# Kernel optimization log

Measured on AMD Instinct MI355X. Metric: run time of the kernel, lower is better.

Reference implementation:

```python
import jax, jax.numpy as jnp
import numpy as np

B, C, H, W = 32, 192, 32, 32
CH, STRIDE = 8, 2
FEAT = CH * (H // STRIDE) * (W // STRIDE)  # 8*16*16 = 2048


def setup_inputs() -> dict:
    key = jax.random.key(0)
    ks = jax.random.split(key, 7)
    inp = jax.random.normal(ks[0], (B, C, H, W), jnp.float32)
    w_left_out = jax.random.normal(ks[1], (B, C, H, W), jnp.float32)
    conv_w = jax.random.normal(ks[2], (CH, C, 3, 3), jnp.float32) * 0.05
    conv_b = jnp.zeros((CH,), jnp.float32)
    # small scale keeps diag(U) moderate so exp(s) stays finite
    lin_w = jax.random.normal(ks[3], (C * C, FEAT), jnp.float32) * 0.01
    lin_b = jax.random.normal(ks[4], (C * C,), jnp.float32) * 0.1
    s_sign = jnp.sign(jax.random.normal(ks[5], (C,), jnp.float32))
    return dict(inp=inp, w_left_out=w_left_out, conv_w=conv_w, conv_b=conv_b,
                lin_w=lin_w, lin_b=lin_b, s_sign=s_sign)


def _cond_net(x, conv_w, conv_b, lin_w, lin_b):
    # Conv2d(C->CH, k=3, stride=2, pad=1) + ReLU + Flatten + Linear(FEAT -> C*C)
    h = jax.lax.conv_general_dilated(
        x, conv_w, window_strides=(STRIDE, STRIDE), padding=((1, 1), (1, 1)),
        dimension_numbers=('NCHW', 'OIHW', 'NCHW'))
    h = jax.nn.relu(h + conv_b[None, :, None, None])
    return h.reshape(x.shape[0], -1) @ lin_w.T + lin_b  # [B, C*C]


def reference(inp, w_left_out, conv_w, conv_b, lin_w, lin_b, s_sign):
    b, c, height, width = inp.shape
    cond = _cond_net(w_left_out, conv_w, conv_b, lin_w, lin_b)
    mats = cond.reshape(b, c, c)
    # batched LU: a = p @ l @ u (scipy convention, unit-diag l)
    p, l, u = jax.vmap(jax.scipy.linalg.lu)(mats)
    s = jnp.diagonal(u, axis1=1, axis2=2)          # [B, C] raw diag(U)
    eye = jnp.eye(c, dtype=inp.dtype)
    l_full = jnp.tril(l, -1) + eye                  # l * l_mask + I
    u_full = jnp.triu(u, 1) + (s_sign[None, :] * jnp.exp(s))[..., None] * eye
    weight = p @ l_full @ u_full                    # [B, C, C]
    # batched 1x1 conv == per-sample GEMM over spatial positions
    out = jnp.einsum('bij,bjhw->bihw', weight, inp)
    log_w = jnp.mean(jnp.sum(s, axis=1))            # sum(w_s) averaged over batch
    log_det = (height * width) * log_w
    return out, log_det
```

## Files before the change

### kernel.cpp

```cpp
#include <hip/hip_runtime.h>
#include <math.h>


#define NFEAT 2048
#define NN    36864

__global__ __launch_bounds__(256) void conv_kernel(const float* __restrict__ w,
                                                   const float* __restrict__ cw,
                                                   float* __restrict__ hpart) {
  int blk = blockIdx.x;
  int b = blk >> 2, cs = blk & 3;
  int tid = threadIdx.x;
  int oy = tid >> 4, ox = tid & 15;
  __shared__ float wlds[8 * 48 * 9];
  for (int idx = tid; idx < 8 * 48 * 9; idx += 256) {
    int ch = idx / 432, rem = idx - ch * 432;
    int c = rem / 9, kk = rem - c * 9;
    wlds[idx] = cw[ch * 1728 + (cs * 48 + c) * 9 + kk];
  }
  __syncthreads();
  float acc[8];
#pragma unroll
  for (int ch = 0; ch < 8; ++ch) acc[ch] = 0.f;
  const float* img0 = w + (((size_t)b * 192 + cs * 48) << 10);
  for (int c = 0; c < 48; ++c) {
    const float* img = img0 + ((size_t)c << 10);
    float iv[9];
#pragma unroll
    for (int ky = 0; ky < 3; ++ky)
#pragma unroll
      for (int kx = 0; kx < 3; ++kx) {
        int iy = 2 * oy - 1 + ky, ix = 2 * ox - 1 + kx;
        bool ok = (iy >= 0) & (iy < 32) & (ix >= 0) & (ix < 32);
        iv[ky * 3 + kx] = ok ? img[iy * 32 + ix] : 0.f;
      }
#pragma unroll
    for (int ch = 0; ch < 8; ++ch) {
      const float* wp = &wlds[(ch * 48 + c) * 9];
      float s = acc[ch];
#pragma unroll
      for (int t = 0; t < 9; ++t) s = fmaf(iv[t], wp[t], s);
      acc[ch] = s;
    }
  }
  size_t base = ((size_t)(cs * 32 + b) << 11) + tid;
#pragma unroll
  for (int ch = 0; ch < 8; ++ch) hpart[base + (ch << 8)] = acc[ch];
}

__global__ __launch_bounds__(256) void hreduce_kernel(const float* __restrict__ hpart,
                                                      const float* __restrict__ cb,
                                                      float* __restrict__ h_t) {
  int g = blockIdx.x * 256 + threadIdx.x;
  int k = g & 2047, b = g >> 11;
  float s = 0.f;
#pragma unroll
  for (int cs = 0; cs < 4; ++cs) s += hpart[(((size_t)(cs * 32 + b)) << 11) + k];
  s += cb[k >> 8];
  s = fmaxf(s, 0.f);
  h_t[((size_t)k << 5) + b] = s;
}

__global__ __launch_bounds__(256) void linear_kernel(const float* __restrict__ h_t,
                                                     const float* __restrict__ lw,
                                                     const float* __restrict__ lb,
                                                     float* __restrict__ mats) {
  __shared__ float Wbuf[64 * 68];
  __shared__ float Hbuf[64 * 36];
  int tid = threadIdx.x;
  int n0 = blockIdx.x << 6;
  int half = tid >> 5;
  int bb = tid & 31;
  int nb = half << 3;
  float accq0[8], accq1[8], accq2[8], accq3[8];
#pragma unroll
  for (int j = 0; j < 8; ++j) { accq0[j] = 0.f; accq1[j] = 0.f; accq2[j] = 0.f; accq3[j] = 0.f; }

#define LIN_CHUNK(ACC)                                                         \
  {                                                                            \
    int koff = kc << 6;                                                        \
    _Pragma("unroll") for (int j = 0; j < 4; ++j) {                            \
      int f = tid + (j << 8);                                                  \
      int row = f >> 4, c4 = (f & 15) << 2;                                    \
      *(float4*)(Wbuf + row * 68 + c4) =                                       \
          *(const float4*)(lw + (size_t)(n0 + row) * 2048 + koff + c4);        \
    }                                                                          \
    _Pragma("unroll") for (int j = 0; j < 2; ++j) {                            \
      int f = tid + (j << 8);                                                  \
      int kr = f >> 3, b4 = (f & 7) << 2;                                      \
      *(float4*)(Hbuf + kr * 36 + b4) =                                        \
          *(const float4*)(h_t + (((size_t)(koff + kr)) << 5) + b4);           \
    }                                                                          \
    __syncthreads();                                                           \
    _Pragma("unroll 4") for (int k4 = 0; k4 < 16; ++k4) {                      \
      int kk = k4 << 2;                                                        \
      float h0 = Hbuf[(kk + 0) * 36 + bb];                                     \
      float h1 = Hbuf[(kk + 1) * 36 + bb];                                     \
      float h2 = Hbuf[(kk + 2) * 36 + bb];                                     \
      float h3 = Hbuf[(kk + 3) * 36 + bb];                                     \
      _Pragma("unroll") for (int j = 0; j < 8; ++j) {                          \
        float4 w4 = *(const float4*)(Wbuf + (nb + j) * 68 + kk);               \
        float s = ACC[j];                                                      \
        s = fmaf(w4.x, h0, s);                                                 \
        s = fmaf(w4.y, h1, s);                                                 \
        s = fmaf(w4.z, h2, s);                                                 \
        s = fmaf(w4.w, h3, s);                                                 \
        ACC[j] = s;                                                            \
      }                                                                        \
    }                                                                          \
    __syncthreads();                                                           \
  }

  for (int kc = 0; kc < 8; ++kc)  LIN_CHUNK(accq0)
  for (int kc = 8; kc < 16; ++kc) LIN_CHUNK(accq1)
  for (int kc = 16; kc < 24; ++kc) LIN_CHUNK(accq2)
  for (int kc = 24; kc < 32; ++kc) LIN_CHUNK(accq3)
#undef LIN_CHUNK

  float o[8];
#pragma unroll
  for (int j = 0; j < 8; ++j)
    o[j] = ((accq0[j] + accq1[j]) + accq2[j]) + accq3[j] + lb[n0 + nb + j];
  float* mp = mats + (size_t)bb * NN + n0 + nb;
  *(float4*)(mp + 0) = make_float4(o[0], o[1], o[2], o[3]);
  *(float4*)(mp + 4) = make_float4(o[4], o[5], o[6], o[7]);
}

#define CAT_(A, B) A##B
#define CAT(A, B) CAT_(A, B)
#define PR_0(R) CAT(pA, R).x
#define PR_1(R) CAT(pA, R).y
#define PR_2(R) CAT(pA, R).z
#define PR_3(R) CAT(pA, R).w
#define PR_4(R) CAT(pB, R).x
#define PR_5(R) CAT(pB, R).y
#define PR_6(R) CAT(pB, R).z
#define PR_7(R) CAT(pB, R).w
#define PR(R, K) CAT(PR_, K)(R)
#define UU_0 uA.x
#define UU_1 uA.y
#define UU_2 uA.z
#define UU_3 uA.w
#define UU_4 uB.x
#define UU_5 uB.y
#define UU_6 uB.z
#define UU_7 uB.w
#define UU(K) CAT(UU_, K)
#define UPDJ(R, J) PR(R, J) = fmaf(-m, UU(J), PR(R, J));
#define TAIL_0(R) UPDJ(R,1) UPDJ(R,2) UPDJ(R,3) UPDJ(R,4) UPDJ(R,5) UPDJ(R,6) UPDJ(R,7)
#define TAIL_1(R) UPDJ(R,2) UPDJ(R,3) UPDJ(R,4) UPDJ(R,5) UPDJ(R,6) UPDJ(R,7)
#define TAIL_2(R) UPDJ(R,3) UPDJ(R,4) UPDJ(R,5) UPDJ(R,6) UPDJ(R,7)
#define TAIL_3(R) UPDJ(R,4) UPDJ(R,5) UPDJ(R,6) UPDJ(R,7)
#define TAIL_4(R) UPDJ(R,5) UPDJ(R,6) UPDJ(R,7)
#define TAIL_5(R) UPDJ(R,6) UPDJ(R,7)
#define TAIL_6(R) UPDJ(R,7)
#define TAIL_7(R)
#define UPDROW(R, KK, kg)                                                      \
  if (CAT(lg, R) > (kg)) {                                                     \
    float m = PR(R, KK) * recip;                                               \
    PR(R, KK) = m;                                                             \
    CAT(TAIL_, KK)(R)                                                          \
  }
#define PSTEP(KK) {                                                            \
  const int kg = kpP + KK;                                                     \
  float bv = -1.f; int br = 0x7fffffff;                                        \
  { float v = fabsf(PR(0,KK)); if (lg0 >= kg && (v > bv || (v == bv && lg0 < br))) { bv = v; br = lg0; } } \
  { float v = fabsf(PR(1,KK)); if (lg1 >= kg && (v > bv || (v == bv && lg1 < br))) { bv = v; br = lg1; } } \
  { float v = fabsf(PR(2,KK)); if (lg2 >= kg && (v > bv || (v == bv && lg2 < br))) { bv = v; br = lg2; } } \
  for (int msk = 1; msk <= 32; msk <<= 1) {                                    \
    float ov = __shfl_xor(bv, msk, 64);                                        \
    int obr = __shfl_xor(br, msk, 64);                                         \
    if (ov > bv || (ov == bv && obr < br)) { bv = ov; br = obr; }              \
  }                                                                            \
  bool own0 = (lg0 == br), own1 = (lg1 == br), own2 = (lg2 == br);             \
  float4 sA = own1 ? pA1 : (own2 ? pA2 : pA0);                                 \
  float4 sB = own1 ? pB1 : (own2 ? pB2 : pB0);                                 \
  int owner = (int)__ffsll(__ballot(own0 | own1 | own2)) - 1;                  \
  float4 uA, uB;                                                               \
  uA.x = __shfl(sA.x, owner); uA.y = __shfl(sA.y, owner);                      \
  uA.z = __shfl(sA.z, owner); uA.w = __shfl(sA.w, owner);                      \
  uB.x = __shfl(sB.x, owner); uB.y = __shfl(sB.y, owner);                      \
  uB.z = __shfl(sB.z, owner); uB.w = __shfl(sB.w, owner);                      \
  float piv = UU(KK);                                                          \
  float recip = 1.0f / piv;                                                    \
  if (tid == 0) {                                                              \
    diagU[kg] = piv;                                                           \
    int t0 = rowmap[kg], t1 = rowmap[br];                                      \
    rowmap[kg] = t1; rowmap[br] = t0;                                          \
  }                                                                            \
  lg0 = (lg0 == kg) ? br : ((lg0 == br) ? kg : lg0);                           \
  lg1 = (lg1 == kg) ? br : ((lg1 == br) ? kg : lg1);                           \
  lg2 = (lg2 == kg) ? br : ((lg2 == br) ? kg : lg2);                           \
  UPDROW(0, KK, kg)                                                            \
  UPDROW(1, KK, kg)                                                            \
  UPDROW(2, KK, kg)                                                            \
}
#define FMA4(D, M, S) {                                                        \
  float mm = (M);                                                              \
  D.x = fmaf(-mm, S.x, D.x); D.y = fmaf(-mm, S.y, D.y);                        \
  D.z = fmaf(-mm, S.z, D.z); D.w = fmaf(-mm, S.w, D.w);                        \
}
#define PANEL(KPV) {                                                           \
  const int kpP = (KPV);                                                       \
  const int pcP = kpP >> 2;                                                    \
  float4 pA0 = As4[tid * 49 + pcP],         pB0 = As4[tid * 49 + pcP + 1];     \
  float4 pA1 = As4[(tid + 64) * 49 + pcP],  pB1 = As4[(tid + 64) * 49 + pcP + 1]; \
  float4 pA2 = As4[(tid + 128) * 49 + pcP], pB2 = As4[(tid + 128) * 49 + pcP + 1]; \
  PSTEP(0) PSTEP(1) PSTEP(2) PSTEP(3) PSTEP(4) PSTEP(5) PSTEP(6) PSTEP(7)     \
  As4[tid * 49 + pcP] = pA0;         As4[tid * 49 + pcP + 1] = pB0;            \
  As4[(tid + 64) * 49 + pcP] = pA1;  As4[(tid + 64) * 49 + pcP + 1] = pB1;     \
  As4[(tid + 128) * 49 + pcP] = pA2; As4[(tid + 128) * 49 + pcP + 1] = pB2;    \
}

__global__ __launch_bounds__(768, 1) void lu_kernel(float* __restrict__ A0,
                                                    const float* __restrict__ ssign,
                                                    float* __restrict__ ssum) {
  __shared__ float4 As4[192 * 49];
  __shared__ int rowmap[192];
  __shared__ float diagU[192];
  __shared__ float4 dval4[48];
  float* dvalf = (float*)dval4;
  int b = blockIdx.x;
  int tid = threadIdx.x;
  float* __restrict__ A = A0 + (size_t)b * NN;

#pragma unroll
  for (int j = 0; j < 12; ++j) {
    int chunk = tid + 768 * j;
    int row = chunk / 48, q = chunk - row * 48;
    As4[row * 49 + q] = *(const float4*)(A + row * 192 + 4 * q);
  }
  for (int i = tid; i < 192; i += 768) rowmap[i] = i;
  __syncthreads();

  int lg0 = tid, lg1 = tid + 64, lg2 = tid + 128;

  if (tid < 64) { PANEL(0) }
  __syncthreads();

  const int qg = tid >> 4;
  const int slot = tid & 15;

  for (int p = 0; p < 23; ++p) {
    const int kp = p << 3;
    const int pc = kp >> 2;
    const int qp1 = pc + 2;

    if (tid >= qp1 && tid < 48) {
      const int q = tid;
      const int ur0 = rowmap[kp + 0], ur1 = rowmap[kp + 1];
      const int ur2 = rowmap[kp + 2], ur3 = rowmap[kp + 3];
      const int ur4 = rowmap[kp + 4], ur5 = rowmap[kp + 5];
      const int ur6 = rowmap[kp + 6], ur7 = rowmap[kp + 7];
      float4 u40 = As4[ur0 * 49 + q], u41 = As4[ur1 * 49 + q];
      float4 u42 = As4[ur2 * 49 + q], u43 = As4[ur3 * 49 + q];
      float4 u44 = As4[ur4 * 49 + q], u45 = As4[ur5 * 49 + q];
      float4 u46 = As4[ur6 * 49 + q], u47 = As4[ur7 * 49 + q];
      { float4 la = As4[ur1 * 49 + pc];
        FMA4(u41, la.x, u40) }
      { float4 la = As4[ur2 * 49 + pc];
        FMA4(u42, la.x, u40) FMA4(u42, la.y, u41) }
      { float4 la = As4[ur3 * 49 + pc];
        FMA4(u43, la.x, u40) FMA4(u43, la.y, u41) FMA4(u43, la.z, u42) }
      { float4 la = As4[ur4 * 49 + pc];
        FMA4(u44, la.x, u40) FMA4(u44, la.y, u41) FMA4(u44, la.z, u42) FMA4(u44, la.w, u43) }
      { float4 la = As4[ur5 * 49 + pc]; float4 lb2 = As4[ur5 * 49 + pc + 1];
        FMA4(u45, la.x, u40) FMA4(u45, la.y, u41) FMA4(u45, la.z, u42) FMA4(u45, la.w, u43)
        FMA4(u45, lb2.x, u44) }
      { float4 la = As4[ur6 * 49 + pc]; float4 lb2 = As4[ur6 * 49 + pc + 1];
        FMA4(u46, la.x, u40) FMA4(u46, la.y, u41) FMA4(u46, la.z, u42) FMA4(u46, la.w, u43)
        FMA4(u46, lb2.x, u44) FMA4(u46, lb2.y, u45) }
      { float4 la = As4[ur7 * 49 + pc]; float4 lb2 = As4[ur7 * 49 + pc + 1];
        FMA4(u47, la.x, u40) FMA4(u47, la.y, u41) FMA4(u47, la.z, u42) FMA4(u47, la.w, u43)
        FMA4(u47, lb2.x, u44) FMA4(u47, lb2.y, u45) FMA4(u47, lb2.z, u46) }
      As4[ur0 * 49 + q] = u40; As4[ur1 * 49 + q] = u41;
      As4[ur2 * 49 + q] = u42; As4[ur3 * 49 + q] = u43;
      As4[ur4 * 49 + q] = u44; As4[ur5 * 49 + q] = u45;
      As4[ur6 * 49 + q] = u46; As4[ur7 * 49 + q] = u47;
    }
    __syncthreads();

    {
      const int col = qp1 + (tid >= 384 ? 1 : 0);
      const int rsl = tid - (tid >= 384 ? 384 : 0);
      const int s = kp + 8 + rsl;
      if (s < 192) {
        const int ua0 = rowmap[kp + 0], ua1 = rowmap[kp + 1];
        const int ua2 = rowmap[kp + 2], ua3 = rowmap[kp + 3];
        const int ua4 = rowmap[kp + 4], ua5 = rowmap[kp + 5];
        const int ua6 = rowmap[kp + 6], ua7 = rowmap[kp + 7];
        float4 u40 = As4[ua0 * 49 + col], u41 = As4[ua1 * 49 + col];
        float4 u42 = As4[ua2 * 49 + col], u43 = As4[ua3 * 49 + col];
        float4 u44 = As4[ua4 * 49 + col], u45 = As4[ua5 * 49 + col];
        float4 u46 = As4[ua6 * 49 + col], u47 = As4[ua7 * 49 + col];
        int phys = rowmap[s];
        float4 la = As4[phys * 49 + pc];
        float4 lb2 = As4[phys * 49 + pc + 1];
        float4 c = As4[phys * 49 + col];
        FMA4(c, la.x, u40) FMA4(c, la.y, u41) FMA4(c, la.z, u42) FMA4(c, la.w, u43)
        FMA4(c, lb2.x, u44) FMA4(c, lb2.y, u45) FMA4(c, lb2.z, u46) FMA4(c, lb2.w, u47)
        As4[phys * 49 + col] = c;
      }
    }
    int php0, php1, php2, php3, php4, php5, php6, php7, php8, php9, php10, php11;
#define SNAP(I) CAT(php, I) = rowmap[slot + (I << 4)];
    SNAP(0) SNAP(1) SNAP(2) SNAP(3) SNAP(4) SNAP(5) SNAP(6)
    SNAP(7) SNAP(8) SNAP(9) SNAP(10) SNAP(11)
#undef SNAP
    __syncthreads();

    if (tid < 64) {
      PANEL(kp + 8)
    } else if (qg >= qp1 + 2) {
      const int q = qg;
      const int ub0 = rowmap[kp + 0], ub1 = rowmap[kp + 1];
      const int ub2 = rowmap[kp + 2], ub3 = rowmap[kp + 3];
      const int ub4 = rowmap[kp + 4], ub5 = rowmap[kp + 5];
      const int ub6 = rowmap[kp + 6], ub7 = rowmap[kp + 7];
      float4 u40 = As4[ub0 * 49 + q], u41 = As4[ub1 * 49 + q];
      float4 u42 = As4[ub2 * 49 + q], u43 = As4[ub3 * 49 + q];
      float4 u44 = As4[ub4 * 49 + q], u45 = As4[ub5 * 49 + q];
      float4 u46 = As4[ub6 * 49 + q], u47 = As4[ub7 * 49 + q];
#define GEMMROW(I) {                                                           \
      int s = slot + (I << 4);                                                 \
      if (s >= kp + 8) {                                                       \
        int phys = CAT(php, I);                                                \
        float4 la = As4[phys * 49 + pc];                                       \
        float4 lb2 = As4[phys * 49 + pc + 1];                                  \
        float4 c = As4[phys * 49 + q];                                         \
        FMA4(c, la.x, u40) FMA4(c, la.y, u41) FMA4(c, la.z, u42) FMA4(c, la.w, u43) \
        FMA4(c, lb2.x, u44) FMA4(c, lb2.y, u45) FMA4(c, lb2.z, u46) FMA4(c, lb2.w, u47) \
        As4[phys * 49 + q] = c;                                                \
      }                                                                        \
    }
      GEMMROW(0) GEMMROW(1) GEMMROW(2) GEMMROW(3) GEMMROW(4) GEMMROW(5)
      GEMMROW(6) GEMMROW(7) GEMMROW(8) GEMMROW(9) GEMMROW(10) GEMMROW(11)
#undef GEMMROW
    }
    __syncthreads();
  }

  if (tid == 0) {
    float s = 0.f;
    for (int i = 0; i < 192; ++i) s += diagU[i];
    ssum[b] = s;
  }
  if (tid < 192) dvalf[tid] = ssign[tid] * expf(diagU[tid]) - diagU[tid];
  __syncthreads();
  {
    const int r = tid >> 2;
    const int tq = tid & 3;
    int i = r;
    int phys = rowmap[r];
    float di = dvalf[i];
    float* __restrict__ G = A + (size_t)phys * 192;
    int qi = i >> 2;
    for (int j = 0; j < 12; ++j) {
      int q = tq + 4 * j;
      if (q > qi) continue;
      float4 g4 = *(float4*)(G + 4 * q);
      float4 a4 = As4[phys * 49 + q];
      float4 d4 = dval4[q];
      if (q == qi) {
        int c0 = 4 * q;
        g4.x = (c0 + 0 < i) ? g4.x + a4.x * d4.x : ((c0 + 0 == i) ? g4.x + di : g4.x);
        g4.y = (c0 + 1 < i) ? g4.y + a4.y * d4.y : ((c0 + 1 == i) ? g4.y + di : g4.y);
        g4.z = (c0 + 2 < i) ? g4.z + a4.z * d4.z : ((c0 + 2 == i) ? g4.z + di : g4.z);
        g4.w = (c0 + 3 < i) ? g4.w + a4.w * d4.w : ((c0 + 3 == i) ? g4.w + di : g4.w);
      } else {
        g4.x += a4.x * d4.x;
        g4.y += a4.y * d4.y;
        g4.z += a4.z * d4.z;
        g4.w += a4.w * d4.w;
      }
      *(float4*)(G + 4 * q) = g4;
    }
  }
}

__global__ __launch_bounds__(256) void out_kernel(const float* __restrict__ wt,
                                                  const float* __restrict__ inp,
                                                  const float* __restrict__ ssum,
                                                  float* __restrict__ out) {
  int blk = blockIdx.x;
  int b = blk / 24, rem = blk % 24;
  int it = rem >> 3, jt = rem & 7;
  int i0 = it << 6, hw0 = jt << 7;
  int tid = threadIdx.x;
  int tx = tid & 31, ty = tid >> 5;
  __shared__ float wlds[64 * 36];
  __shared__ float xlds[32 * 128];
  const float* wb = wt + (size_t)b * NN;
  const float* xb = inp + (((size_t)b * 192) << 10);
  float acc[8][4];
#pragma unroll
  for (int r = 0; r < 8; ++r)
#pragma unroll
    for (int c = 0; c < 4; ++c) acc[r][c] = 0.f;
  for (int kc = 0; kc < 6; ++kc) {
    __syncthreads();
#pragma unroll
    for (int j = 0; j < 2; ++j) {
      int f4 = tid + (j << 8);
      int row = f4 >> 3, c4 = (f4 & 7) << 2;
      float4 v = *(const float4*)(wb + (size_t)(i0 + row) * 192 + (kc << 5) + c4);
      *(float4*)(wlds + row * 36 + c4) = v;
    }
#pragma unroll
    for (int j = 0; j < 4; ++j) {
      int f4 = tid + (j << 8);
      int row = f4 >> 5, c4 = (f4 & 31) << 2;
      float4 v = *(const float4*)(xb + (((size_t)(kc << 5) + row) << 10) + hw0 + c4);
      *(float4*)(xlds + (row << 7) + c4) = v;
    }
    __syncthreads();
#pragma unroll 4
    for (int k = 0; k < 32; ++k) {
      float4 xv = *(const float4*)(xlds + (k << 7) + (tx << 2));
      float wr[8];
#pragma unroll
      for (int r = 0; r < 8; ++r) wr[r] = wlds[(ty * 8 + r) * 36 + k];
#pragma unroll
      for (int r = 0; r < 8; ++r) {
        acc[r][0] = fmaf(wr[r], xv.x, acc[r][0]);
        acc[r][1] = fmaf(wr[r], xv.y, acc[r][1]);
        acc[r][2] = fmaf(wr[r], xv.z, acc[r][2]);
        acc[r][3] = fmaf(wr[r], xv.w, acc[r][3]);
      }
    }
  }
  float* ob = out + (((size_t)b * 192 + i0 + ty * 8) << 10) + hw0 + (tx << 2);
#pragma unroll
  for (int r = 0; r < 8; ++r) {
    float4 v = make_float4(acc[r][0], acc[r][1], acc[r][2], acc[r][3]);
    *(float4*)(ob + ((size_t)r << 10)) = v;
  }
  if (blk == 0 && tid == 0) {
    float s = 0.f;
    for (int i = 0; i < 32; ++i) s += ssum[i];
    out[6291456] = 32.f * s;
  }
}

extern "C" void kernel_launch(void* const* d_in, const int* in_sizes, int n_in,
                              void* d_out, int out_size, void* d_ws, size_t ws_size,
                              hipStream_t stream) {
  const float* inp = (const float*)d_in[0];
  const float* wlo = (const float*)d_in[1];
  const float* cw  = (const float*)d_in[2];
  const float* cb  = (const float*)d_in[3];
  const float* lw  = (const float*)d_in[4];
  const float* lb  = (const float*)d_in[5];
  const float* ss  = (const float*)d_in[6];
  float* out = (float*)d_out;
  float* ws = (float*)d_ws;
  float* hpart = ws;
  float* h_t   = ws + 262144;
  float* mats  = ws + 327680;
  float* ssum  = ws + 1507328;
  hipLaunchKernelGGL(conv_kernel,    dim3(128), dim3(256), 0, stream, wlo, cw, hpart);
  hipLaunchKernelGGL(hreduce_kernel, dim3(256), dim3(256), 0, stream, hpart, cb, h_t);
  hipLaunchKernelGGL(linear_kernel,  dim3(576), dim3(256), 0, stream, h_t, lw, lb, mats);
  hipLaunchKernelGGL(lu_kernel,      dim3(32),  dim3(768), 0, stream, mats, ss, ssum);
  hipLaunchKernelGGL(out_kernel,     dim3(768), dim3(256), 0, stream, mats, inp, ssum, out);
}
```

Before: 476.7 us.

## Double-buffer linear kernel tiles and compute two batch columns per thread

The linear GEMM kernel now prefetches the next K chunk from global memory into registers while computing on the current shared-memory buffer, using two LDS buffers and one barrier per step. Blocks shrink to 128 threads, each computing two batch columns, which doubles register-level reuse of the W float4 loads. The W rows get a skewed padding to reduce bank conflicts. In exchange it uses more registers per thread and more LDS per block, which may reduce occupancy on a kernel that is largely bound by streaming the large weight matrix.

```diff
diff --git a/kernel.cpp b/kernel.cpp
--- a/kernel.cpp
+++ b/kernel.cpp
@@ -61,69 +61,93 @@
   h_t[((size_t)k << 5) + b] = s;
 }
 
-__global__ __launch_bounds__(256) void linear_kernel(const float* __restrict__ h_t,
+#define WROW(r) ((r) * 68 + (((r) >> 3) << 2))
+__global__ __launch_bounds__(128) void linear_kernel(const float* __restrict__ h_t,
                                                      const float* __restrict__ lw,
                                                      const float* __restrict__ lb,
                                                      float* __restrict__ mats) {
-  __shared__ float Wbuf[64 * 68];
-  __shared__ float Hbuf[64 * 36];
+  __shared__ float Wbuf[2][64 * 68 + 32];
+  __shared__ float Hbuf[2][64 * 36];
   int tid = threadIdx.x;
   int n0 = blockIdx.x << 6;
-  int half = tid >> 5;
-  int bb = tid & 31;
-  int nb = half << 3;
-  float accq0[8], accq1[8], accq2[8], accq3[8];
-#pragma unroll
-  for (int j = 0; j < 8; ++j) { accq0[j] = 0.f; accq1[j] = 0.f; accq2[j] = 0.f; accq3[j] = 0.f; }
-
-#define LIN_CHUNK(ACC)                                                         \
-  {                                                                            \
-    int koff = kc << 6;                                                        \
+  int bp = tid & 15;
+  int nsub = tid >> 4;
+  int nb = nsub << 3;
+  int bb0 = bp << 1;
+  float4 wst[8];
+  float4 hst[4];
+  float accq0[16], accq1[16], accq2[16], accq3[16];
+#pragma unroll
+  for (int j = 0; j < 16; ++j) { accq0[j] = 0.f; accq1[j] = 0.f; accq2[j] = 0.f; accq3[j] = 0.f; }
+
+#define LIN_LOADG(KC)                                                          \
+  { int koff = (KC) << 6;                                                      \
+    _Pragma("unroll") for (int j = 0; j < 8; ++j) {                            \
+      int f = tid + (j << 7); int row = f >> 4, c4 = (f & 15) << 2;            \
+      wst[j] = *(const float4*)(lw + (size_t)(n0 + row) * 2048 + koff + c4); } \
     _Pragma("unroll") for (int j = 0; j < 4; ++j) {                            \
-      int f = tid + (j << 8);                                                  \
-      int row = f >> 4, c4 = (f & 15) << 2;                                    \
-      *(float4*)(Wbuf + row * 68 + c4) =                                       \
-          *(const float4*)(lw + (size_t)(n0 + row) * 2048 + koff + c4);        \
-    }                                                                          \
-    _Pragma("unroll") for (int j = 0; j < 2; ++j) {                            \
-      int f = tid + (j << 8);                                                  \
-      int kr = f >> 3, b4 = (f & 7) << 2;                                      \
-      *(float4*)(Hbuf + kr * 36 + b4) =                                        \
-          *(const float4*)(h_t + (((size_t)(koff + kr)) << 5) + b4);           \
-    }                                                                          \
-    __syncthreads();                                                           \
-    _Pragma("unroll 4") for (int k4 = 0; k4 < 16; ++k4) {                      \
+      int f = tid + (j << 7); int kr = f >> 3, b4 = (f & 7) << 2;              \
+      hst[j] = *(const float4*)(h_t + (((size_t)(koff + kr)) << 5) + b4); } }
+
+#define LIN_STORE(BUF)                                                         \
+  { _Pragma("unroll") for (int j = 0; j < 8; ++j) {                            \
+      int f = tid + (j << 7); int row = f >> 4, c4 = (f & 15) << 2;            \
+      *(float4*)(Wbuf[BUF] + WROW(row) + c4) = wst[j]; }                       \
+    _Pragma("unroll") for (int j = 0; j < 4; ++j) {                            \
+      int f = tid + (j << 7); int kr = f >> 3, b4 = (f & 7) << 2;              \
+      *(float4*)(Hbuf[BUF] + kr * 36 + b4) = hst[j]; } }
+
+#define LIN_COMPUTE(BUF, ACC)                                                  \
+  { const float* Wb = Wbuf[BUF]; const float* Hb = Hbuf[BUF];                  \
+    _Pragma("unroll 2") for (int k4 = 0; k4 < 16; ++k4) {                      \
       int kk = k4 << 2;                                                        \
-      float h0 = Hbuf[(kk + 0) * 36 + bb];                                     \
-      float h1 = Hbuf[(kk + 1) * 36 + bb];                                     \
-      float h2 = Hbuf[(kk + 2) * 36 + bb];                                     \
-      float h3 = Hbuf[(kk + 3) * 36 + bb];                                     \
+      float h00 = Hb[(kk + 0) * 36 + bb0], h01 = Hb[(kk + 1) * 36 + bb0];      \
+      float h02 = Hb[(kk + 2) * 36 + bb0], h03 = Hb[(kk + 3) * 36 + bb0];      \
+      float h10 = Hb[(kk + 0) * 36 + bb0 + 1], h11 = Hb[(kk + 1) * 36 + bb0 + 1]; \
+      float h12 = Hb[(kk + 2) * 36 + bb0 + 1], h13 = Hb[(kk + 3) * 36 + bb0 + 1]; \
       _Pragma("unroll") for (int j = 0; j < 8; ++j) {                          \
-        float4 w4 = *(const float4*)(Wbuf + (nb + j) * 68 + kk);               \
-        float s = ACC[j];                                                      \
-        s = fmaf(w4.x, h0, s);                                                 \
-        s = fmaf(w4.y, h1, s);                                                 \
-        s = fmaf(w4.z, h2, s);                                                 \
-        s = fmaf(w4.w, h3, s);                                                 \
-        ACC[j] = s;                                                            \
+        float4 w4 = *(const float4*)(Wb + WROW(nb + j) + kk);                  \
+        float s0 = ACC[2 * j], s1 = ACC[2 * j + 1];                            \
+        s0 = fmaf(w4.x, h00, s0); s0 = fmaf(w4.y, h01, s0);                    \
+        s0 = fmaf(w4.z, h02, s0); s0 = fmaf(w4.w, h03, s0);                    \
+        s1 = fmaf(w4.x, h10, s1); s1 = fmaf(w4.y, h11, s1);                    \
+        s1 = fmaf(w4.z, h12, s1); s1 = fmaf(w4.w, h13, s1);                    \
+        ACC[2 * j] = s0; ACC[2 * j + 1] = s1;                                  \
       }                                                                        \
-    }                                                                          \
-    __syncthreads();                                                           \
-  }
-
-  for (int kc = 0; kc < 8; ++kc)  LIN_CHUNK(accq0)
-  for (int kc = 8; kc < 16; ++kc) LIN_CHUNK(accq1)
-  for (int kc = 16; kc < 24; ++kc) LIN_CHUNK(accq2)
-  for (int kc = 24; kc < 32; ++kc) LIN_CHUNK(accq3)
-#undef LIN_CHUNK
-
-  float o[8];
-#pragma unroll
-  for (int j = 0; j < 8; ++j)
-    o[j] = ((accq0[j] + accq1[j]) + accq2[j]) + accq3[j] + lb[n0 + nb + j];
-  float* mp = mats + (size_t)bb * NN + n0 + nb;
-  *(float4*)(mp + 0) = make_float4(o[0], o[1], o[2], o[3]);
-  *(float4*)(mp + 4) = make_float4(o[4], o[5], o[6], o[7]);
+    } }
+
+#define LIN_STEP(ACC)                                                          \
+  { int buf = kc & 1;                                                          \
+    if (kc < 31) { LIN_LOADG(kc + 1) }                                         \
+    LIN_COMPUTE(buf, ACC)                                                      \
+    if (kc < 31) { LIN_STORE(buf ^ 1) }                                        \
+    __syncthreads(); }
+
+  LIN_LOADG(0)
+  LIN_STORE(0)
+  __syncthreads();
+  for (int kc = 0; kc < 8; ++kc)   LIN_STEP(accq0)
+  for (int kc = 8; kc < 16; ++kc)  LIN_STEP(accq1)
+  for (int kc = 16; kc < 24; ++kc) LIN_STEP(accq2)
+  for (int kc = 24; kc < 32; ++kc) LIN_STEP(accq3)
+#undef LIN_STEP
+#undef LIN_COMPUTE
+#undef LIN_STORE
+#undef LIN_LOADG
+
+  float o[16];
+#pragma unroll
+  for (int j = 0; j < 8; ++j) {
+    float bias = lb[n0 + nb + j];
+    o[2 * j]     = ((accq0[2 * j] + accq1[2 * j]) + accq2[2 * j]) + accq3[2 * j] + bias;
+    o[2 * j + 1] = ((accq0[2 * j + 1] + accq1[2 * j + 1]) + accq2[2 * j + 1]) + accq3[2 * j + 1] + bias;
+  }
+  float* mp0 = mats + (size_t)bb0 * NN + n0 + nb;
+  float* mp1 = mats + (size_t)(bb0 + 1) * NN + n0 + nb;
+  *(float4*)(mp0 + 0) = make_float4(o[0], o[2], o[4], o[6]);
+  *(float4*)(mp0 + 4) = make_float4(o[8], o[10], o[12], o[14]);
+  *(float4*)(mp1 + 0) = make_float4(o[1], o[3], o[5], o[7]);
+  *(float4*)(mp1 + 4) = make_float4(o[9], o[11], o[13], o[15]);
 }
 
 #define CAT_(A, B) A##B
@@ -460,7 +484,7 @@
   float* ssum  = ws + 1507328;
   hipLaunchKernelGGL(conv_kernel,    dim3(128), dim3(256), 0, stream, wlo, cw, hpart);
   hipLaunchKernelGGL(hreduce_kernel, dim3(256), dim3(256), 0, stream, hpart, cb, h_t);
-  hipLaunchKernelGGL(linear_kernel,  dim3(576), dim3(256), 0, stream, h_t, lw, lb, mats);
+  hipLaunchKernelGGL(linear_kernel,  dim3(576), dim3(128), 0, stream, h_t, lw, lb, mats);
   hipLaunchKernelGGL(lu_kernel,      dim3(32),  dim3(768), 0, stream, mats, ss, ssum);
   hipLaunchKernelGGL(out_kernel,     dim3(768), dim3(256), 0, stream, mats, inp, ssum, out);
 }
```

After: 500.6 us. 5.0% more time.
